# Kernel tuning notes

Measured on AMD Instinct MI355X. Metric: run time of the kernel, lower is better.

The kernel has to match this reference:

```python
import jax, jax.numpy as jnp
import numpy as np

WINDOW_SIZE = 7
CT_SIZE = 2
NUM_HEADS = 8


def _relative_position_index(ws: int) -> np.ndarray:
    coords = np.arange(ws)
    grid = np.stack(np.meshgrid(coords, coords, indexing='ij'))  # (2, ws, ws)
    flat = grid.reshape(2, -1)                                   # (2, ws*ws)
    rel = flat[:, :, None] - flat[:, None, :]                    # (2, M, M)
    rel = rel.transpose(1, 2, 0).copy()                          # (M, M, 2)
    rel[..., 0] += ws - 1
    rel[..., 1] += ws - 1
    rel[..., 0] *= 2 * ws - 1
    return rel.sum(-1).reshape(-1)                               # (M*M,)

REL_POS_INDEX = _relative_position_index(WINDOW_SIZE)


def setup_inputs() -> dict:
    key = jax.random.key(0)
    ks = jax.random.split(key, 6)
    B, N, C = 4096, WINDOW_SIZE ** 2 + CT_SIZE ** 2, 256
    x = jax.random.normal(ks[0], (B, N, C), dtype=jnp.float32)
    qkv_w = jax.random.normal(ks[1], (3 * C, C), dtype=jnp.float32) * 0.02
    qkv_b = jax.random.normal(ks[2], (3 * C,), dtype=jnp.float32) * 0.02
    proj_w = jax.random.normal(ks[3], (C, C), dtype=jnp.float32) * 0.02
    proj_b = jax.random.normal(ks[4], (C,), dtype=jnp.float32) * 0.02
    tbl = (2 * WINDOW_SIZE - 1) ** 2
    rel_bias_table = jax.random.normal(ks[5], (tbl, NUM_HEADS), dtype=jnp.float32) * 0.02
    return {"x": x, "qkv_w": qkv_w, "qkv_b": qkv_b, "proj_w": proj_w,
            "proj_b": proj_b, "rel_bias_table": rel_bias_table}


def reference(x, qkv_w, qkv_b, proj_w, proj_b, rel_bias_table):
    B, N, C = x.shape
    H = NUM_HEADS
    hd = C // H
    scale = hd ** (-0.5)
    M = WINDOW_SIZE ** 2                      # local window tokens (49)
    pad = N - M                               # carrier tokens (4)

    # qkv projection -> (3, B, H, N, hd)
    qkv = (x @ qkv_w.T + qkv_b).reshape(B, N, 3, H, hd).transpose(2, 0, 3, 1, 4)
    q, k, v = qkv[0], qkv[1], qkv[2]

    attn = jnp.einsum('bhnd,bhmd->bhnm', q, k) * scale   # (B, H, N, N)

    # relative position bias on the window-token block only (bottom-right)
    bias = rel_bias_table[REL_POS_INDEX].reshape(M, M, H)  # (49, 49, H)
    bias = bias.transpose(2, 0, 1)                         # (H, 49, 49)
    bias = jnp.pad(bias, ((0, 0), (pad, 0), (pad, 0)))     # (H, N, N)
    attn = attn + bias[None]

    attn = jax.nn.softmax(attn, axis=-1)
    out = jnp.einsum('bhnm,bhmd->bhnd', attn, v)           # (B, H, N, hd)
    out = out.transpose(0, 2, 1, 3).reshape(B, N, C)
    return out @ proj_w.T + proj_b
```

## Files before the change

### kernel.cpp

```cpp
#include <hip/hip_runtime.h>

typedef __attribute__((ext_vector_type(8))) short vbf8;
typedef __attribute__((ext_vector_type(4))) float vf4;

#define NT 53
#define CD 256
#define NH 8
#define HIMG 65536
#define PROJ_OFF 524288
#define QBS_OFF  655360
#define ATTN_OFF 1048576

#define LOG2E 1.4426950408889634f
#define SCALE 0.17677669529663687f

__device__ __forceinline__ unsigned pk2(float a, float b) {
    unsigned r;
    asm("v_cvt_pk_bf16_f32 %0, %1, %2" : "=v"(r) : "v"(a), "v"(b));
    return r;
}

__device__ __forceinline__ vbf8 xpose(vf4 A, vf4 B, int odd) {
    unsigned A0 = pk2(A[0], A[1]), A1 = pk2(A[2], A[3]);
    unsigned B0 = pk2(B[0], B[1]), B1 = pk2(B[2], B[3]);
    asm("v_permlane32_swap_b32 %0, %1" : "+v"(A0), "+v"(B0));
    asm("v_permlane32_swap_b32 %0, %1" : "+v"(A1), "+v"(B1));
    unsigned s0 = (unsigned)__shfl_xor((int)B0, 16, 64);
    unsigned s1 = (unsigned)__shfl_xor((int)B1, 16, 64);
    unsigned t0 = (unsigned)__shfl_xor((int)A0, 16, 64);
    unsigned t1 = (unsigned)__shfl_xor((int)A1, 16, 64);
    union { unsigned u[4]; vbf8 v; } r;
    r.u[0] = odd ? s0 : A0;
    r.u[1] = odd ? s1 : A1;
    r.u[2] = odd ? B0 : t0;
    r.u[3] = odd ? B1 : t1;
    return r.v;
}

__device__ __forceinline__ void gl_lds16(const void* g, void* l) {
    __builtin_amdgcn_global_load_lds((const __attribute__((address_space(1))) unsigned*)g,
                                     (__attribute__((address_space(3))) unsigned*)l, 16, 0, 0);
}

__global__ void k0_prep(const float* __restrict__ qkv_w, const float* __restrict__ tbl,
                        const float* __restrict__ proj_w, const float* __restrict__ qkv_b,
                        char* __restrict__ ws)
{
    const int u = (int)blockIdx.x * 256 + (int)threadIdx.x;
    if (u < 24576) {
        const int h = u / 3072, rem = u - h * 3072;
        const int sec = rem >> 10, rem2 = rem & 1023;
        const int row = rem2 >> 5, seg = rem2 & 31;
        const float* src = qkv_w + ((size_t)(sec * 256 + h * 32 + row)) * 256 + seg * 8;
        const float sc = (sec == 0) ? SCALE * LOG2E : 1.0f;
        vf4 a = *(const vf4*)src;
        vf4 b = *(const vf4*)(src + 4);
        union { unsigned w[4]; vbf8 v; } r;
        r.w[0] = pk2(a[0] * sc, a[1] * sc); r.w[1] = pk2(a[2] * sc, a[3] * sc);
        r.w[2] = pk2(b[0] * sc, b[1] * sc); r.w[3] = pk2(b[2] * sc, b[3] * sc);
        char* dst = ws + (size_t)h * HIMG + sec * 16384 + row * 512 + ((seg * 16) ^ ((row & 7) << 4));
        *(vbf8*)dst = r.v;
    } else if (u < 32768) {
        const int t = u - 24576;
        const int h = t >> 10, rem = t & 1023;
        const int q = rem >> 4, seg = rem & 15;
        vf4 r;
        #pragma unroll
        for (int e = 0; e < 4; ++e) {
            const int key = seg * 4 + e;
            float bv;
            if (key >= NT) bv = -1e30f;
            else if (key < 4 || q < 4 || q >= NT) bv = 0.0f;
            else {
                const int i = q - 4, j = key - 4;
                const int idx = ((i / 7) - (j / 7) + 6) * 13 + ((i % 7) - (j % 7) + 6);
                bv = tbl[idx * NH + h] * LOG2E;
            }
            r[e] = bv;
        }
        char* dst = ws + (size_t)h * HIMG + 49152 + q * 256 + ((seg * 16) ^ ((q & 7) << 4));
        *(vf4*)dst = r;
    } else if (u < 40960) {
        const int t = u - 32768;
        const int kc = t >> 11, rem = t & 2047;
        const int row = rem >> 3, seg = rem & 7;
        const float* src = proj_w + (size_t)row * 256 + kc * 64 + seg * 8;
        vf4 a = *(const vf4*)src;
        vf4 b = *(const vf4*)(src + 4);
        union { unsigned w[4]; vbf8 v; } r;
        r.w[0] = pk2(a[0], a[1]); r.w[1] = pk2(a[2], a[3]);
        r.w[2] = pk2(b[0], b[1]); r.w[3] = pk2(b[2], b[3]);
        char* dst = ws + PROJ_OFF + kc * 32768 + row * 128 + ((seg * 16) ^ ((row & 7) << 4));
        *(vbf8*)dst = r.v;
    } else if (u < 41152) {
        const int i = (u - 40960) * 4;
        float* dst = (float*)(ws + QBS_OFF);
        #pragma unroll
        for (int e = 0; e < 4; ++e) {
            const int j = i + e;
            dst[j] = qkv_b[j] * (j < 256 ? SCALE * LOG2E : 1.0f);
        }
    }
}

__launch_bounds__(512, 2)
__global__ void k1_fused(const float* __restrict__ x,
                         const float* __restrict__ qbs,
                         const char* __restrict__ himg,
                         short* __restrict__ attnH,
                         int win0, int Mtot)
{
    __shared__ char lds[2][HIMG];

    const int tid  = threadIdx.x;
    const int wave = tid >> 6;
    const int lane = tid & 63;
    const int c    = lane & 15;
    const int g    = lane >> 4;
    const int odd  = g & 1;
    const int win  = win0 + (int)blockIdx.x * 8 + wave;

    auto stage = [&](int h, int buf) {
        const char* src = himg + (size_t)h * HIMG;
        #pragma unroll
        for (int i = 0; i < 8; ++i) {
            const int u = tid + i * 512;
            gl_lds16(src + (size_t)u * 16, &lds[buf][(i * 512 + wave * 64) * 16]);
        }
    };

    stage(0, 0);

    vbf8 xf[4][8];
    {
        const float* xb = x + (size_t)win * (NT * CD);
        #pragma unroll
        for (int mt = 0; mt < 4; ++mt) {
            const int row = mt * 16 + c;
            const float* src = xb + row * CD + g * 8;
            #pragma unroll
            for (int ks = 0; ks < 8; ++ks) {
                vbf8 z = {0, 0, 0, 0, 0, 0, 0, 0};
                if (row < NT) {
                    vf4 a = *(const vf4*)(src + ks * 32);
                    vf4 b = *(const vf4*)(src + ks * 32 + 4);
                    union { unsigned w[4]; vbf8 v; } r;
                    r.w[0] = pk2(a[0], a[1]); r.w[1] = pk2(a[2], a[3]);
                    r.w[2] = pk2(b[0], b[1]); r.w[3] = pk2(b[2], b[3]);
                    z = r.v;
                }
                xf[mt][ks] = z;
            }
        }
    }
    __syncthreads();

    #pragma unroll 1
    for (int h = 0; h < NH; ++h) {
        const int cur = h & 1;
        if (h < 7) stage(h + 1, cur ^ 1);
        const char* wb = lds[cur];

        auto rdW = [&](int sec, int rr, int ks) -> vbf8 {
            const int byte = sec * 16384 + rr * 512 + (((ks * 64) + g * 16) ^ ((rr & 7) << 4));
            return *(const vbf8*)(wb + byte);
        };

        vf4 qa[2][4];
        #pragma unroll
        for (int mt = 0; mt < 2; ++mt) {
            vf4 bi = *(const vf4*)(qbs + h * 32 + mt * 16 + g * 4);
            #pragma unroll
            for (int nt = 0; nt < 4; ++nt) qa[mt][nt] = bi;
        }
        __builtin_amdgcn_s_setprio(1);
        #pragma unroll
        for (int mt = 0; mt < 2; ++mt)
            #pragma unroll
            for (int ks = 0; ks < 8; ++ks) {
                vbf8 wf = rdW(0, mt * 16 + c, ks);
                #pragma unroll
                for (int nt = 0; nt < 4; ++nt)
                    qa[mt][nt] = __builtin_amdgcn_mfma_f32_16x16x32_bf16(wf, xf[nt][ks], qa[mt][nt], 0, 0, 0);
            }
        __builtin_amdgcn_s_setprio(0);
        vbf8 qf[4];
        #pragma unroll
        for (int nt = 0; nt < 4; ++nt) qf[nt] = xpose(qa[0][nt], qa[1][nt], odd);

        vf4 ka[2][4];
        #pragma unroll
        for (int mt = 0; mt < 2; ++mt) {
            vf4 bi = *(const vf4*)(qbs + 256 + h * 32 + mt * 16 + g * 4);
            #pragma unroll
            for (int nt = 0; nt < 4; ++nt) ka[mt][nt] = bi;
        }
        __builtin_amdgcn_s_setprio(1);
        #pragma unroll
        for (int mt = 0; mt < 2; ++mt)
            #pragma unroll
            for (int ks = 0; ks < 8; ++ks) {
                vbf8 wf = rdW(1, mt * 16 + c, ks);
                #pragma unroll
                for (int nt = 0; nt < 4; ++nt)
                    ka[mt][nt] = __builtin_amdgcn_mfma_f32_16x16x32_bf16(wf, xf[nt][ks], ka[mt][nt], 0, 0, 0);
            }
        __builtin_amdgcn_s_setprio(0);
        vbf8 kf[4];
        #pragma unroll
        for (int nt = 0; nt < 4; ++nt) kf[nt] = xpose(ka[0][nt], ka[1][nt], odd);

        vbf8 vfr[2][2];
        {
            vf4 va[4][2];
            #pragma unroll
            for (int nv = 0; nv < 2; ++nv) {
                const float vb = qbs[512 + h * 32 + nv * 16 + c];
                vf4 bi = {vb, vb, vb, vb};
                #pragma unroll
                for (int mt = 0; mt < 4; ++mt) va[mt][nv] = bi;
            }
            __builtin_amdgcn_s_setprio(1);
            #pragma unroll
            for (int nv = 0; nv < 2; ++nv)
                #pragma unroll
                for (int ks = 0; ks < 8; ++ks) {
                    vbf8 wf = rdW(2, nv * 16 + c, ks);
                    #pragma unroll
                    for (int mt = 0; mt < 4; ++mt)
                        va[mt][nv] = __builtin_amdgcn_mfma_f32_16x16x32_bf16(xf[mt][ks], wf, va[mt][nv], 0, 0, 0);
                }
            __builtin_amdgcn_s_setprio(0);
            #pragma unroll
            for (int nv = 0; nv < 2; ++nv)
                #pragma unroll
                for (int ks = 0; ks < 2; ++ks)
                    vfr[nv][ks] = xpose(va[2 * ks][nv], va[2 * ks + 1][nv], odd);
        }

        const char* bb = wb + 49152;
        vf4 st[4][4];
        #pragma unroll
        for (int nq = 0; nq < 4; ++nq) {
            const int row = nq * 16 + c;
            #pragma unroll
            for (int mk = 0; mk < 4; ++mk)
                st[mk][nq] = *(const vf4*)(bb + row * 256 + (((mk * 64) + g * 16) ^ ((row & 7) << 4)));
        }
        __builtin_amdgcn_s_setprio(1);
        #pragma unroll
        for (int mk = 0; mk < 4; ++mk)
            #pragma unroll
            for (int nq = 0; nq < 4; ++nq)
                st[mk][nq] = __builtin_amdgcn_mfma_f32_16x16x32_bf16(kf[mk], qf[nq], st[mk][nq], 0, 0, 0);
        __builtin_amdgcn_s_setprio(0);

        float linv[4];
        #pragma unroll
        for (int nq = 0; nq < 4; ++nq) {
            float mx = -3e38f;
            #pragma unroll
            for (int mk = 0; mk < 4; ++mk)
                #pragma unroll
                for (int r = 0; r < 4; ++r) mx = fmaxf(mx, st[mk][nq][r]);
            mx = fmaxf(mx, __shfl_xor(mx, 16, 64));
            mx = fmaxf(mx, __shfl_xor(mx, 32, 64));
            float sum = 0.f;
            #pragma unroll
            for (int mk = 0; mk < 4; ++mk)
                #pragma unroll
                for (int r = 0; r < 4; ++r) {
                    float p = exp2f(st[mk][nq][r] - mx);
                    st[mk][nq][r] = p;
                    sum += p;
                }
            sum += __shfl_xor(sum, 16, 64);
            sum += __shfl_xor(sum, 32, 64);
            linv[nq] = 1.f / sum;
        }

        vbf8 pfr[4][2];
        #pragma unroll
        for (int nq = 0; nq < 4; ++nq)
            #pragma unroll
            for (int ks = 0; ks < 2; ++ks)
                pfr[nq][ks] = xpose(st[2 * ks][nq], st[2 * ks + 1][nq], odd);

        vf4 ot[2][4];
        #pragma unroll
        for (int mt = 0; mt < 2; ++mt)
            #pragma unroll
            for (int nq = 0; nq < 4; ++nq) { vf4 z = {0.f,0.f,0.f,0.f}; ot[mt][nq] = z; }
        __builtin_amdgcn_s_setprio(1);
        #pragma unroll
        for (int ks = 0; ks < 2; ++ks)
            #pragma unroll
            for (int mt = 0; mt < 2; ++mt)
                #pragma unroll
                for (int nq = 0; nq < 4; ++nq)
                    ot[mt][nq] = __builtin_amdgcn_mfma_f32_16x16x32_bf16(vfr[mt][ks], pfr[nq][ks], ot[mt][nq], 0, 0, 0);
        __builtin_amdgcn_s_setprio(0);

        #pragma unroll
        for (int nq = 0; nq < 4; ++nq) {
            vf4 A = ot[0][nq], B = ot[1][nq];
            #pragma unroll
            for (int r = 0; r < 4; ++r) { A[r] *= linv[nq]; B[r] *= linv[nq]; }
            vbf8 o = xpose(A, B, odd);
            const int qq = nq * 16 + c;
            if (qq < NT) {
                const int mrow = (win - win0) * NT + qq;
                *(vbf8*)(attnH + ((size_t)h * Mtot + mrow) * 32 + g * 8) = o;
            }
        }
        __syncthreads();
    }
}

__launch_bounds__(256, 4)
__global__ void k2_proj(const short* __restrict__ attnH,
                        const char* __restrict__ projimg,
                        const float* __restrict__ proj_b,
                        float* __restrict__ out,
                        int Mtot)
{
    __shared__ char a_lds[8192];
    __shared__ char b_lds[32768];

    const int tid  = threadIdx.x;
    const int wave = tid >> 6;
    const int lane = tid & 63;
    const int c    = lane & 15;
    const int g    = lane >> 4;
    const int m0   = (int)blockIdx.x * 64;

    vf4 acc[4][4];
    #pragma unroll
    for (int mt = 0; mt < 4; ++mt)
        #pragma unroll
        for (int nt = 0; nt < 4; ++nt) { vf4 z = {0.f,0.f,0.f,0.f}; acc[mt][nt] = z; }

    for (int kc = 0; kc < 4; ++kc) {
        __syncthreads();
        #pragma unroll
        for (int rr = 0; rr < 2; ++rr) {
            const int u    = tid + rr * 256;
            const int row  = u >> 3;
            const int sub  = u & 7;
            const int subs = sub ^ (row & 7);
            const int head = kc * 2 + (subs >> 2);
            const int kk   = (subs & 3) * 8;
            int mrow = m0 + row; if (mrow >= Mtot) mrow = Mtot - 1;
            gl_lds16(attnH + ((size_t)head * Mtot + mrow) * 32 + kk,
                     &a_lds[(rr * 256 + wave * 64) * 16]);
        }
        #pragma unroll
        for (int it = 0; it < 8; ++it) {
            const int u = tid + it * 256;
            gl_lds16(projimg + (size_t)kc * 32768 + (size_t)u * 16,
                     &b_lds[(it * 256 + wave * 64) * 16]);
        }
        __syncthreads();
        #pragma unroll
        for (int ksub = 0; ksub < 2; ++ksub) {
            vbf8 af[4], bfr[4];
            #pragma unroll
            for (int mt = 0; mt < 4; ++mt) {
                const int row = mt * 16 + c;
                af[mt] = *(const vbf8*)(a_lds + row * 128 + (((ksub * 64) + g * 16) ^ ((row & 7) << 4)));
            }
            #pragma unroll
            for (int nt = 0; nt < 4; ++nt) {
                const int row = wave * 64 + nt * 16 + c;
                bfr[nt] = *(const vbf8*)(b_lds + row * 128 + (((ksub * 64) + g * 16) ^ ((row & 7) << 4)));
            }
            #pragma unroll
            for (int mt = 0; mt < 4; ++mt)
                #pragma unroll
                for (int nt = 0; nt < 4; ++nt)
                    acc[mt][nt] = __builtin_amdgcn_mfma_f32_16x16x32_bf16(af[mt], bfr[nt], acc[mt][nt], 0, 0, 0);
        }
    }
    #pragma unroll
    for (int nt = 0; nt < 4; ++nt) {
        const int n = wave * 64 + nt * 16 + c;
        const float pb = proj_b[n];
        #pragma unroll
        for (int mt = 0; mt < 4; ++mt)
            #pragma unroll
            for (int r = 0; r < 4; ++r) {
                const int m = m0 + mt * 16 + g * 4 + r;
                if (m < Mtot) out[(size_t)m * 256 + n] = acc[mt][nt][r] + pb;
            }
    }
}

extern "C" void kernel_launch(void* const* d_in, const int* in_sizes, int n_in,
                              void* d_out, int out_size, void* d_ws, size_t ws_size,
                              hipStream_t stream)
{
    const float* x      = (const float*)d_in[0];
    const float* qkv_w  = (const float*)d_in[1];
    const float* qkv_b  = (const float*)d_in[2];
    const float* proj_w = (const float*)d_in[3];
    const float* proj_b = (const float*)d_in[4];
    const float* tbl    = (const float*)d_in[5];
    float* out = (float*)d_out;
    char* ws   = (char*)d_ws;

    k0_prep<<<161, 256, 0, stream>>>(qkv_w, tbl, proj_w, qkv_b, ws);

    short* attn = (short*)(ws + ATTN_OFF);
    const float* qbs = (const float*)(ws + QBS_OFF);
    const size_t bpw = (size_t)NT * 32 * 2 * NH;
    long cw = (ws_size > ATTN_OFF) ? (long)((ws_size - ATTN_OFF) / bpw) : 8;
    if (cw > 4096) cw = 4096;
    cw &= ~7L;
    if (cw < 8) cw = 8;
    for (int start = 0; start < 4096; start += (int)cw) {
        int count = 4096 - start; if (count > (int)cw) count = (int)cw;
        const int Mc = count * NT;
        k1_fused<<<count / 8, 512, 0, stream>>>(x, qbs, ws, attn, start, Mc);
        k2_proj<<<(Mc + 63) / 64, 256, 0, stream>>>(attn, ws + PROJ_OFF, proj_b,
                                                    out + (size_t)start * NT * CD, Mc);
    }
    (void)in_sizes; (void)n_in; (void)out_size;
}
```

Baseline: 336.9 us.

## Remap k1 to one window per block with heads split across waves

The fused attention kernel changes its mapping. It goes from eight windows per 512-thread block, with every wave looping over all heads and per-head weights double-buffered in LDS, to one window per 256-thread block with each wave handling two heads. The input tile is converted to bf16 into a swizzled LDS buffer and shared by the four waves. Weights and bias are pre-packed into MFMA fragment order so each lane reads them straight from global memory. This removes the LDS weight staging and the per-head barriers and lowers register pressure. The cost is repeated global or L2 reads of the weight image per block and more blocks in total.

```diff
diff --git a/kernel.cpp b/kernel.cpp
--- a/kernel.cpp
+++ b/kernel.cpp
@@ -48,26 +48,32 @@
 {
     const int u = (int)blockIdx.x * 256 + (int)threadIdx.x;
     if (u < 24576) {
-        const int h = u / 3072, rem = u - h * 3072;
-        const int sec = rem >> 10, rem2 = rem & 1023;
-        const int row = rem2 >> 5, seg = rem2 & 31;
-        const float* src = qkv_w + ((size_t)(sec * 256 + h * 32 + row)) * 256 + seg * 8;
-        const float sc = (sec == 0) ? SCALE * LOG2E : 1.0f;
+        const int h = u / 3072, r = u - h * 3072;
+        const int F = r >> 6, l = r & 63;
+        const int c = l & 15, g = l >> 4;
+        const int ks = F & 7;
+        int srcrow; float sc = 1.0f;
+        if (F < 16)      { srcrow = h * 32 + (F >> 3) * 16 + c; sc = SCALE * LOG2E; }
+        else if (F < 32) { srcrow = 256 + h * 32 + ((F >> 3) - 2) * 16 + c; }
+        else             { srcrow = 512 + h * 32 + ((F - 32) >> 3) * 16 + c; }
+        const float* src = qkv_w + (size_t)srcrow * 256 + ks * 32 + g * 8;
         vf4 a = *(const vf4*)src;
         vf4 b = *(const vf4*)(src + 4);
-        union { unsigned w[4]; vbf8 v; } r;
-        r.w[0] = pk2(a[0] * sc, a[1] * sc); r.w[1] = pk2(a[2] * sc, a[3] * sc);
-        r.w[2] = pk2(b[0] * sc, b[1] * sc); r.w[3] = pk2(b[2] * sc, b[3] * sc);
-        char* dst = ws + (size_t)h * HIMG + sec * 16384 + row * 512 + ((seg * 16) ^ ((row & 7) << 4));
-        *(vbf8*)dst = r.v;
+        union { unsigned w[4]; vbf8 v; } rv;
+        rv.w[0] = pk2(a[0] * sc, a[1] * sc); rv.w[1] = pk2(a[2] * sc, a[3] * sc);
+        rv.w[2] = pk2(b[0] * sc, b[1] * sc); rv.w[3] = pk2(b[2] * sc, b[3] * sc);
+        *(vbf8*)(ws + (size_t)h * HIMG + F * 1024 + l * 16) = rv.v;
     } else if (u < 32768) {
         const int t = u - 24576;
-        const int h = t >> 10, rem = t & 1023;
-        const int q = rem >> 4, seg = rem & 15;
-        vf4 r;
+        const int h = t >> 10, r2 = t & 1023;
+        const int F = r2 >> 6, l = r2 & 63;
+        const int mk = F >> 2, nq = F & 3;
+        const int c = l & 15, g = l >> 4;
+        vf4 rv;
         #pragma unroll
         for (int e = 0; e < 4; ++e) {
-            const int key = seg * 4 + e;
+            const int key = mk * 16 + g * 4 + e;
+            const int q   = nq * 16 + c;
             float bv;
             if (key >= NT) bv = -1e30f;
             else if (key < 4 || q < 4 || q >= NT) bv = 0.0f;
@@ -76,10 +82,9 @@
                 const int idx = ((i / 7) - (j / 7) + 6) * 13 + ((i % 7) - (j % 7) + 6);
                 bv = tbl[idx * NH + h] * LOG2E;
             }
-            r[e] = bv;
-        }
-        char* dst = ws + (size_t)h * HIMG + 49152 + q * 256 + ((seg * 16) ^ ((q & 7) << 4));
-        *(vf4*)dst = r;
+            rv[e] = bv;
+        }
+        *(vf4*)(ws + (size_t)h * HIMG + 49152 + F * 1024 + l * 16) = rv;
     } else if (u < 40960) {
         const int t = u - 32768;
         const int kc = t >> 11, rem = t & 2047;
@@ -87,11 +92,11 @@
         const float* src = proj_w + (size_t)row * 256 + kc * 64 + seg * 8;
         vf4 a = *(const vf4*)src;
         vf4 b = *(const vf4*)(src + 4);
-        union { unsigned w[4]; vbf8 v; } r;
-        r.w[0] = pk2(a[0], a[1]); r.w[1] = pk2(a[2], a[3]);
-        r.w[2] = pk2(b[0], b[1]); r.w[3] = pk2(b[2], b[3]);
+        union { unsigned w[4]; vbf8 v; } rv;
+        rv.w[0] = pk2(a[0], a[1]); rv.w[1] = pk2(a[2], a[3]);
+        rv.w[2] = pk2(b[0], b[1]); rv.w[3] = pk2(b[2], b[3]);
         char* dst = ws + PROJ_OFF + kc * 32768 + row * 128 + ((seg * 16) ^ ((row & 7) << 4));
-        *(vbf8*)dst = r.v;
+        *(vbf8*)dst = rv.v;
     } else if (u < 41152) {
         const int i = (u - 40960) * 4;
         float* dst = (float*)(ws + QBS_OFF);
@@ -103,14 +108,14 @@
     }
 }
 
-__launch_bounds__(512, 2)
+__launch_bounds__(256, 4)
 __global__ void k1_fused(const float* __restrict__ x,
                          const float* __restrict__ qbs,
-                         const char* __restrict__ himg,
+                         const char* __restrict__ wimg,
                          short* __restrict__ attnH,
                          int win0, int Mtot)
 {
-    __shared__ char lds[2][HIMG];
+    __shared__ char xlds[32768];
 
     const int tid  = threadIdx.x;
     const int wave = tid >> 6;
@@ -118,97 +123,83 @@
     const int c    = lane & 15;
     const int g    = lane >> 4;
     const int odd  = g & 1;
-    const int win  = win0 + (int)blockIdx.x * 8 + wave;
-
-    auto stage = [&](int h, int buf) {
-        const char* src = himg + (size_t)h * HIMG;
-        #pragma unroll
-        for (int i = 0; i < 8; ++i) {
-            const int u = tid + i * 512;
-            gl_lds16(src + (size_t)u * 16, &lds[buf][(i * 512 + wave * 64) * 16]);
-        }
-    };
-
-    stage(0, 0);
-
-    vbf8 xf[4][8];
+    const int win  = win0 + (int)blockIdx.x;
+
     {
         const float* xb = x + (size_t)win * (NT * CD);
         #pragma unroll
+        for (int i = 0; i < 8; ++i) {
+            const int u   = tid + i * 256;
+            const int row = u >> 5, seg = u & 31;
+            const int F   = (row >> 4) * 8 + (seg >> 2);
+            const int dl  = (seg & 3) * 16 + (row & 15);
+            char* dst = xlds + F * 1024 + (dl ^ (F & 7)) * 16;
+            if (row < NT) {
+                const float* s = xb + row * CD + seg * 8;
+                vf4 a = *(const vf4*)s;
+                vf4 b = *(const vf4*)(s + 4);
+                union { unsigned w[4]; vbf8 v; } r;
+                r.w[0] = pk2(a[0], a[1]); r.w[1] = pk2(a[2], a[3]);
+                r.w[2] = pk2(b[0], b[1]); r.w[3] = pk2(b[2], b[3]);
+                *(vbf8*)dst = r.v;
+            } else {
+                vbf8 z = {0, 0, 0, 0, 0, 0, 0, 0};
+                *(vbf8*)dst = z;
+            }
+        }
+    }
+    __syncthreads();
+
+    auto rdX = [&](int F) -> vbf8 {
+        return *(const vbf8*)(xlds + F * 1024 + ((lane ^ (F & 7)) * 16));
+    };
+
+    #pragma unroll 1
+    for (int hh = 0; hh < 2; ++hh) {
+        const int h = wave + hh * 4;
+        const char* wh = wimg + (size_t)h * HIMG;
+
+        auto ldW = [&](int F) -> vbf8 {
+            return *(const vbf8*)(wh + F * 1024 + lane * 16);
+        };
+
+        vf4 qk[4][4];
+        #pragma unroll
         for (int mt = 0; mt < 4; ++mt) {
-            const int row = mt * 16 + c;
-            const float* src = xb + row * CD + g * 8;
-            #pragma unroll
-            for (int ks = 0; ks < 8; ++ks) {
-                vbf8 z = {0, 0, 0, 0, 0, 0, 0, 0};
-                if (row < NT) {
-                    vf4 a = *(const vf4*)(src + ks * 32);
-                    vf4 b = *(const vf4*)(src + ks * 32 + 4);
-                    union { unsigned w[4]; vbf8 v; } r;
-                    r.w[0] = pk2(a[0], a[1]); r.w[1] = pk2(a[2], a[3]);
-                    r.w[2] = pk2(b[0], b[1]); r.w[3] = pk2(b[2], b[3]);
-                    z = r.v;
-                }
-                xf[mt][ks] = z;
-            }
-        }
-    }
-    __syncthreads();
-
-    #pragma unroll 1
-    for (int h = 0; h < NH; ++h) {
-        const int cur = h & 1;
-        if (h < 7) stage(h + 1, cur ^ 1);
-        const char* wb = lds[cur];
-
-        auto rdW = [&](int sec, int rr, int ks) -> vbf8 {
-            const int byte = sec * 16384 + rr * 512 + (((ks * 64) + g * 16) ^ ((rr & 7) << 4));
-            return *(const vbf8*)(wb + byte);
-        };
-
-        vf4 qa[2][4];
-        #pragma unroll
-        for (int mt = 0; mt < 2; ++mt) {
-            vf4 bi = *(const vf4*)(qbs + h * 32 + mt * 16 + g * 4);
-            #pragma unroll
-            for (int nt = 0; nt < 4; ++nt) qa[mt][nt] = bi;
+            const float* bsrc = (mt < 2) ? (qbs + h * 32 + mt * 16 + g * 4)
+                                         : (qbs + 256 + h * 32 + (mt - 2) * 16 + g * 4);
+            vf4 bi = *(const vf4*)bsrc;
+            #pragma unroll
+            for (int nt = 0; nt < 4; ++nt) qk[mt][nt] = bi;
         }
         __builtin_amdgcn_s_setprio(1);
         #pragma unroll
-        for (int mt = 0; mt < 2; ++mt)
-            #pragma unroll
-            for (int ks = 0; ks < 8; ++ks) {
-                vbf8 wf = rdW(0, mt * 16 + c, ks);
-                #pragma unroll
-                for (int nt = 0; nt < 4; ++nt)
-                    qa[mt][nt] = __builtin_amdgcn_mfma_f32_16x16x32_bf16(wf, xf[nt][ks], qa[mt][nt], 0, 0, 0);
-            }
+        for (int ks = 0; ks < 8; ++ks) {
+            vbf8 w0 = ldW(ks), w1 = ldW(8 + ks), w2 = ldW(16 + ks), w3 = ldW(24 + ks);
+            vbf8 x0 = rdX(ks), x1 = rdX(8 + ks), x2 = rdX(16 + ks), x3 = rdX(24 + ks);
+            qk[0][0] = __builtin_amdgcn_mfma_f32_16x16x32_bf16(w0, x0, qk[0][0], 0, 0, 0);
+            qk[0][1] = __builtin_amdgcn_mfma_f32_16x16x32_bf16(w0, x1, qk[0][1], 0, 0, 0);
+            qk[0][2] = __builtin_amdgcn_mfma_f32_16x16x32_bf16(w0, x2, qk[0][2], 0, 0, 0);
+            qk[0][3] = __builtin_amdgcn_mfma_f32_16x16x32_bf16(w0, x3, qk[0][3], 0, 0, 0);
+            qk[1][0] = __builtin_amdgcn_mfma_f32_16x16x32_bf16(w1, x0, qk[1][0], 0, 0, 0);
+            qk[1][1] = __builtin_amdgcn_mfma_f32_16x16x32_bf16(w1, x1, qk[1][1], 0, 0, 0);
+            qk[1][2] = __builtin_amdgcn_mfma_f32_16x16x32_bf16(w1, x2, qk[1][2], 0, 0, 0);
+            qk[1][3] = __builtin_amdgcn_mfma_f32_16x16x32_bf16(w1, x3, qk[1][3], 0, 0, 0);
+            qk[2][0] = __builtin_amdgcn_mfma_f32_16x16x32_bf16(w2, x0, qk[2][0], 0, 0, 0);
+            qk[2][1] = __builtin_amdgcn_mfma_f32_16x16x32_bf16(w2, x1, qk[2][1], 0, 0, 0);
+            qk[2][2] = __builtin_amdgcn_mfma_f32_16x16x32_bf16(w2, x2, qk[2][2], 0, 0, 0);
+            qk[2][3] = __builtin_amdgcn_mfma_f32_16x16x32_bf16(w2, x3, qk[2][3], 0, 0, 0);
+            qk[3][0] = __builtin_amdgcn_mfma_f32_16x16x32_bf16(w3, x0, qk[3][0], 0, 0, 0);
+            qk[3][1] = __builtin_amdgcn_mfma_f32_16x16x32_bf16(w3, x1, qk[3][1], 0, 0, 0);
+            qk[3][2] = __builtin_amdgcn_mfma_f32_16x16x32_bf16(w3, x2, qk[3][2], 0, 0, 0);
+            qk[3][3] = __builtin_amdgcn_mfma_f32_16x16x32_bf16(w3, x3, qk[3][3], 0, 0, 0);
+        }
         __builtin_amdgcn_s_setprio(0);
-        vbf8 qf[4];
-        #pragma unroll
-        for (int nt = 0; nt < 4; ++nt) qf[nt] = xpose(qa[0][nt], qa[1][nt], odd);
-
-        vf4 ka[2][4];
-        #pragma unroll
-        for (int mt = 0; mt < 2; ++mt) {
-            vf4 bi = *(const vf4*)(qbs + 256 + h * 32 + mt * 16 + g * 4);
-            #pragma unroll
-            for (int nt = 0; nt < 4; ++nt) ka[mt][nt] = bi;
-        }
-        __builtin_amdgcn_s_setprio(1);
-        #pragma unroll
-        for (int mt = 0; mt < 2; ++mt)
-            #pragma unroll
-            for (int ks = 0; ks < 8; ++ks) {
-                vbf8 wf = rdW(1, mt * 16 + c, ks);
-                #pragma unroll
-                for (int nt = 0; nt < 4; ++nt)
-                    ka[mt][nt] = __builtin_amdgcn_mfma_f32_16x16x32_bf16(wf, xf[nt][ks], ka[mt][nt], 0, 0, 0);
-            }
-        __builtin_amdgcn_s_setprio(0);
-        vbf8 kf[4];
-        #pragma unroll
-        for (int nt = 0; nt < 4; ++nt) kf[nt] = xpose(ka[0][nt], ka[1][nt], odd);
+        vbf8 qf[4], kf[4];
+        #pragma unroll
+        for (int nt = 0; nt < 4; ++nt) qf[nt] = xpose(qk[0][nt], qk[1][nt], odd);
+        #pragma unroll
+        for (int nt = 0; nt < 4; ++nt) kf[nt] = xpose(qk[2][nt], qk[3][nt], odd);
 
         vbf8 vfr[2][2];
         {
@@ -222,31 +213,32 @@
             }
             __builtin_amdgcn_s_setprio(1);
             #pragma unroll
+            for (int ks = 0; ks < 8; ++ks) {
+                vbf8 v0 = ldW(32 + ks), v1 = ldW(40 + ks);
+                vbf8 x0 = rdX(ks), x1 = rdX(8 + ks), x2 = rdX(16 + ks), x3 = rdX(24 + ks);
+                va[0][0] = __builtin_amdgcn_mfma_f32_16x16x32_bf16(x0, v0, va[0][0], 0, 0, 0);
+                va[1][0] = __builtin_amdgcn_mfma_f32_16x16x32_bf16(x1, v0, va[1][0], 0, 0, 0);
+                va[2][0] = __builtin_amdgcn_mfma_f32_16x16x32_bf16(x2, v0, va[2][0], 0, 0, 0);
+                va[3][0] = __builtin_amdgcn_mfma_f32_16x16x32_bf16(x3, v0, va[3][0], 0, 0, 0);
+                va[0][1] = __builtin_amdgcn_mfma_f32_16x16x32_bf16(x0, v1, va[0][1], 0, 0, 0);
+                va[1][1] = __builtin_amdgcn_mfma_f32_16x16x32_bf16(x1, v1, va[1][1], 0, 0, 0);
+                va[2][1] = __builtin_amdgcn_mfma_f32_16x16x32_bf16(x2, v1, va[2][1], 0, 0, 0);
+                va[3][1] = __builtin_amdgcn_mfma_f32_16x16x32_bf16(x3, v1, va[3][1], 0, 0, 0);
+            }
+            __builtin_amdgcn_s_setprio(0);
+            #pragma unroll
             for (int nv = 0; nv < 2; ++nv)
                 #pragma unroll
-                for (int ks = 0; ks < 8; ++ks) {
-                    vbf8 wf = rdW(2, nv * 16 + c, ks);
-                    #pragma unroll
-                    for (int mt = 0; mt < 4; ++mt)
-                        va[mt][nv] = __builtin_amdgcn_mfma_f32_16x16x32_bf16(xf[mt][ks], wf, va[mt][nv], 0, 0, 0);
-                }
-            __builtin_amdgcn_s_setprio(0);
-            #pragma unroll
-            for (int nv = 0; nv < 2; ++nv)
-                #pragma unroll
-                for (int ks = 0; ks < 2; ++ks)
-                    vfr[nv][ks] = xpose(va[2 * ks][nv], va[2 * ks + 1][nv], odd);
-        }
-
-        const char* bb = wb + 49152;
+                for (int kp = 0; kp < 2; ++kp)
+                    vfr[nv][kp] = xpose(va[2 * kp][nv], va[2 * kp + 1][nv], odd);
+        }
+
         vf4 st[4][4];
         #pragma unroll
-        for (int nq = 0; nq < 4; ++nq) {
-            const int row = nq * 16 + c;
-            #pragma unroll
-            for (int mk = 0; mk < 4; ++mk)
-                st[mk][nq] = *(const vf4*)(bb + row * 256 + (((mk * 64) + g * 16) ^ ((row & 7) << 4)));
-        }
+        for (int mk = 0; mk < 4; ++mk)
+            #pragma unroll
+            for (int nq = 0; nq < 4; ++nq)
+                st[mk][nq] = *(const vf4*)(wh + 49152 + (mk * 4 + nq) * 1024 + lane * 16);
         __builtin_amdgcn_s_setprio(1);
         #pragma unroll
         for (int mk = 0; mk < 4; ++mk)
@@ -283,8 +275,8 @@
         #pragma unroll
         for (int nq = 0; nq < 4; ++nq)
             #pragma unroll
-            for (int ks = 0; ks < 2; ++ks)
-                pfr[nq][ks] = xpose(st[2 * ks][nq], st[2 * ks + 1][nq], odd);
+            for (int kp = 0; kp < 2; ++kp)
+                pfr[nq][kp] = xpose(st[2 * kp][nq], st[2 * kp + 1][nq], odd);
 
         vf4 ot[2][4];
         #pragma unroll
@@ -293,12 +285,12 @@
             for (int nq = 0; nq < 4; ++nq) { vf4 z = {0.f,0.f,0.f,0.f}; ot[mt][nq] = z; }
         __builtin_amdgcn_s_setprio(1);
         #pragma unroll
-        for (int ks = 0; ks < 2; ++ks)
+        for (int kp = 0; kp < 2; ++kp)
             #pragma unroll
             for (int mt = 0; mt < 2; ++mt)
                 #pragma unroll
                 for (int nq = 0; nq < 4; ++nq)
-                    ot[mt][nq] = __builtin_amdgcn_mfma_f32_16x16x32_bf16(vfr[mt][ks], pfr[nq][ks], ot[mt][nq], 0, 0, 0);
+                    ot[mt][nq] = __builtin_amdgcn_mfma_f32_16x16x32_bf16(vfr[mt][kp], pfr[nq][kp], ot[mt][nq], 0, 0, 0);
         __builtin_amdgcn_s_setprio(0);
 
         #pragma unroll
@@ -313,7 +305,6 @@
                 *(vbf8*)(attnH + ((size_t)h * Mtot + mrow) * 32 + g * 8) = o;
             }
         }
-        __syncthreads();
     }
 }
 
@@ -413,14 +404,13 @@
     short* attn = (short*)(ws + ATTN_OFF);
     const float* qbs = (const float*)(ws + QBS_OFF);
     const size_t bpw = (size_t)NT * 32 * 2 * NH;
-    long cw = (ws_size > ATTN_OFF) ? (long)((ws_size - ATTN_OFF) / bpw) : 8;
+    long cw = (ws_size > ATTN_OFF) ? (long)((ws_size - ATTN_OFF) / bpw) : 1;
     if (cw > 4096) cw = 4096;
-    cw &= ~7L;
-    if (cw < 8) cw = 8;
+    if (cw < 1) cw = 1;
     for (int start = 0; start < 4096; start += (int)cw) {
         int count = 4096 - start; if (count > (int)cw) count = (int)cw;
         const int Mc = count * NT;
-        k1_fused<<<count / 8, 512, 0, stream>>>(x, qbs, ws, attn, start, Mc);
+        k1_fused<<<count, 256, 0, stream>>>(x, qbs, ws, attn, start, Mc);
         k2_proj<<<(Mc + 63) / 64, 256, 0, stream>>>(attn, ws + PROJ_OFF, proj_b,
                                                     out + (size_t)start * NT * CD, Mc);
     }
```

Result: slower. 559.3 us (+66.0%).
